# Optimization experiments

Measured on AMD Instinct MI355X. Metric: run time of the kernel, lower is better.

## Reference

```python
import jax, jax.numpy as jnp
import numpy as np

EPS = 1e-5
HEADS = 4
DIMK = 16
DIMU = 4
R = 23


def _bn_eval(x, g, b):
    # BatchNorm2d in eval mode with running_mean=0, running_var=1
    return x * (g / np.sqrt(1.0 + EPS))[None, :, None, None] + b[None, :, None, None]


def _conv1x1(x, w):
    # w: (O, C) from a Conv2d(C, O, 1) weight
    return jnp.einsum('bchw,oc->bohw', x, w)


def _lambda_layer(x, wq, wk, wv, qg, qb, vg, vb, pw, pb):
    B, C, H, W = x.shape
    n = H * W
    V = wv.shape[0] // DIMU  # dim_out // heads
    q = _bn_eval(_conv1x1(x, wq), qg, qb).reshape(B, HEADS, DIMK, n)
    k = jax.nn.softmax(_conv1x1(x, wk).reshape(B, DIMU, DIMK, n), axis=-1)
    v = _bn_eval(_conv1x1(x, wv), vg, vb).reshape(B, DIMU, V, n)
    # content lambda: (B, k, v)
    lam_c = jnp.einsum('bukn,buvn->bkv', k, v)
    y_c = jnp.einsum('bhkn,bkv->bhvn', q, lam_c)
    # position lambdas: Conv3d(u, k, (1, R, R)) == 2D conv over (H, W) with v folded into batch
    v5 = v.reshape(B, DIMU, V, H, W).transpose(0, 2, 1, 3, 4).reshape(B * V, DIMU, H, W)
    p = R // 2
    lp = jax.lax.conv_general_dilated(v5, pw, (1, 1), [(p, p), (p, p)],
                                      dimension_numbers=('NCHW', 'OIHW', 'NCHW'))
    lp = lp + pb[None, :, None, None]
    lam_p = lp.reshape(B, V, DIMK, H, W).transpose(0, 2, 1, 3, 4).reshape(B, DIMK, V, n)
    y_p = jnp.einsum('bhkn,bkvn->bhvn', q, lam_p)
    return (y_c + y_p).reshape(B, HEADS * V, H, W)


def _group_norm(x, g, b, groups=8):
    B, C, H, W = x.shape
    xr = x.reshape(B, groups, C // groups, H, W)
    m = xr.mean(axis=(2, 3, 4), keepdims=True)
    var = xr.var(axis=(2, 3, 4), keepdims=True)
    xn = ((xr - m) / jnp.sqrt(var + EPS)).reshape(B, C, H, W)
    return xn * g[None, :, None, None] + b[None, :, None, None]


def setup_inputs() -> dict:
    key = jax.random.key(0)
    B, C, H, W = 4, 64, 192, 192
    V = C // HEADS
    d = {'x': jax.random.normal(jax.random.fold_in(key, 0), (B, C, H, W), jnp.float32)}
    i = 1
    for l in (1, 2, 3):
        for nm, shape, kind in [
            ('wq', (HEADS * DIMK, C), 'w'), ('wk', (DIMU * DIMK, C), 'w'), ('wv', (DIMU * V, C), 'w'),
            ('qg', (HEADS * DIMK,), 'ones'), ('qb', (HEADS * DIMK,), 'zeros'),
            ('vg', (DIMU * V,), 'ones'), ('vb', (DIMU * V,), 'zeros'),
            ('pw', (DIMK, DIMU, R, R), 'w'), ('pb', (DIMK,), 'zeros')]:
            if kind == 'w':
                d['l%d_%s' % (l, nm)] = jax.random.normal(jax.random.fold_in(key, i), shape, jnp.float32) * 0.05
            elif kind == 'ones':
                d['l%d_%s' % (l, nm)] = jnp.ones(shape, jnp.float32)
            else:
                d['l%d_%s' % (l, nm)] = jnp.zeros(shape, jnp.float32)
            i += 1
    d['gn1_g'] = jnp.ones((C,), jnp.float32); d['gn1_b'] = jnp.zeros((C,), jnp.float32)
    d['gn3_g'] = jnp.ones((C,), jnp.float32); d['gn3_b'] = jnp.zeros((C,), jnp.float32)
    d['cw'] = jax.random.normal(jax.random.fold_in(key, 99), (C, C), jnp.float32) * 0.01
    d['cb'] = jnp.zeros((C,), jnp.float32)
    return d


def reference(x,
              l1_wq, l1_wk, l1_wv, l1_qg, l1_qb, l1_vg, l1_vb, l1_pw, l1_pb,
              l2_wq, l2_wk, l2_wv, l2_qg, l2_qb, l2_vg, l2_vb, l2_pw, l2_pb,
              l3_wq, l3_wk, l3_wv, l3_qg, l3_qb, l3_vg, l3_vb, l3_pw, l3_pb,
              gn1_g, gn1_b, gn3_g, gn3_b, cw, cb):
    out = _lambda_layer(x, l1_wq, l1_wk, l1_wv, l1_qg, l1_qb, l1_vg, l1_vb, l1_pw, l1_pb)
    out = _group_norm(out, gn1_g, gn1_b)
    out = _lambda_layer(out, l2_wq, l2_wk, l2_wv, l2_qg, l2_qb, l2_vg, l2_vb, l2_pw, l2_pb)
    out = _group_norm(out, gn1_g, gn1_b)  # original code reuses gn1 here (gn2 unused)
    out = _lambda_layer(out, l3_wq, l3_wk, l3_wv, l3_qg, l3_qb, l3_vg, l3_vb, l3_pw, l3_pb)
    out = _group_norm(out, gn3_g, gn3_b)
    out = _conv1x1(out, cw) + cb[None, :, None, None]
    return out * 0.2 + x
```

## Files before the change

kernel.cpp:

```cpp
#include <hip/hip_runtime.h>

typedef unsigned short USH;
typedef __attribute__((ext_vector_type(8))) short bf16x8;
typedef __attribute__((ext_vector_type(4))) float f32x4;

#define MFMA16(a,b,c) __builtin_amdgcn_mfma_f32_16x16x32_bf16((a),(b),(c),0,0,0)

#define BB 4
#define HH 192
#define NN 36864
#define NTOT 147456
#define CSTR 120

__device__ __forceinline__ float bf2f(USH h) {
    union { unsigned int u; float f; } v; v.u = ((unsigned int)h) << 16; return v.f;
}
__device__ __forceinline__ USH f2bf(float f) {
    union { float f; unsigned int u; } v; v.f = f;
    unsigned int u = v.u;
    return (USH)((u + 0x7FFFu + ((u >> 16) & 1u)) >> 16);
}

struct PrepArgs {
    const float* wq[3]; const float* wk[3]; const float* wv[3];
    const float* qg[3]; const float* qb[3]; const float* vg[3]; const float* vb[3];
    const float* pw[3]; const float* cw;
};
__global__ void prep_all_k(PrepArgs pa, USH* __restrict__ apc, USH* __restrict__ apq,
                           float* __restrict__ biasq, USH* __restrict__ apf) {
    int bid = blockIdx.x, tid = threadIdx.x;
    if (bid < 552) {
        int L = bid / 184, cb = bid - L * 184;
        int t = cb * 256 + tid;
        if (t < 736 * 64) {
            const float* pw = pa.pw[L];
            USH* ap = apc + (size_t)L * 376832;
            int lane = t & 63, cg = t >> 6;
            int dy = cg % 23; int ru = cg / 23; int u = ru & 3; int r = ru >> 2;
            int kk = lane & 15, q8 = (lane >> 4) * 8;
            for (int j = 0; j < 8; ++j) {
                int k = q8 + j, dx = k - r;
                USH w = 0;
                if (dx >= 0 && dx < 23) w = f2bf(pw[((kk * 4 + u) * 23 + dy) * 23 + dx]);
                ap[t * 8 + j] = w;
            }
        }
    } else if (bid < 570) {
        int idx = bid - 552; int L = idx / 6; int qblk = idx - L * 6;
        int t = qblk * 256 + tid;
        USH* apl = apq + (size_t)L * 12288;
        float* bl = biasq + L * 192;
        if (t < 1536) {
            int lane = t & 63, chunk = t >> 6;
            int mt = chunk >> 1, kc = chunk & 1;
            int o = mt * 16 + (lane & 15);
            int c0 = kc * 32 + (lane >> 4) * 8;
            float scale; const float* wrow;
            if (o < 64)       { scale = pa.qg[L][o]       * rsqrtf(1.0f + 1e-5f); wrow = pa.wq[L] + o * 64; }
            else if (o < 128) { scale = 1.0f;                                     wrow = pa.wk[L] + (o - 64) * 64; }
            else              { scale = pa.vg[L][o - 128] * rsqrtf(1.0f + 1e-5f); wrow = pa.wv[L] + (o - 128) * 64; }
            for (int j = 0; j < 8; ++j) apl[t * 8 + j] = f2bf(wrow[c0 + j] * scale);
        }
        if (t < 192) {
            float bvv;
            if (t < 64) bvv = pa.qb[L][t]; else if (t < 128) bvv = 0.0f; else bvv = pa.vb[L][t - 128];
            bl[t] = bvv;
        }
    } else {
        int t = (bid - 570) * 256 + tid;
        if (t < 512) {
            int lane = t & 63, chunk = t >> 6;
            int mt = chunk >> 1, kc = chunk & 1;
            int o = mt * 16 + (lane & 15);
            int c0 = kc * 32 + (lane >> 4) * 8;
            for (int j = 0; j < 8; ++j) apf[t * 8 + j] = f2bf(pa.cw[o * 64 + c0 + j]);
        }
    }
}

__global__ __launch_bounds__(256) void x_qkv_k(
    const float* __restrict__ xin, const bf16x8* __restrict__ apre, const float* __restrict__ bias,
    USH* __restrict__ qT, USH* __restrict__ kbuf, USH* __restrict__ vbuf) {
    __shared__ float tf[64][65];
    const int bid = blockIdx.x; const int b = bid / 576; const int nt = bid - b * 576; const int n0 = nt * 64;
    const int tid = threadIdx.x, lane = tid & 63, wq = tid >> 6;
    const int nl = lane & 15, quad = lane >> 4;
    bf16x8 afr[24];
    #pragma unroll
    for (int i = 0; i < 24; ++i) afr[i] = apre[i * 64 + lane];
    #pragma unroll
    for (int p = 0; p < 16; ++p) {
        int idx = p * 256 + tid; int c = idx >> 6, nn = idx & 63;
        tf[nn][c] = xin[((size_t)b * 64 + c) * NN + n0 + nn];
    }
    __syncthreads();
    bf16x8 b0, b1;
    #pragma unroll
    for (int j = 0; j < 8; ++j) {
        b0[j] = (short)f2bf(tf[wq * 16 + nl][quad * 8 + j]);
        b1[j] = (short)f2bf(tf[wq * 16 + nl][32 + quad * 8 + j]);
    }
    const int n = n0 + wq * 16 + nl;
    #pragma unroll
    for (int mt = 0; mt < 12; ++mt) {
        f32x4 acc = {0.f, 0.f, 0.f, 0.f};
        acc = MFMA16(afr[mt * 2 + 0], b0, acc);
        acc = MFMA16(afr[mt * 2 + 1], b1, acc);
        int o0 = mt * 16 + quad * 4;
        float4 bs = *(const float4*)(bias + o0);
        float v0 = acc[0] + bs.x, v1 = acc[1] + bs.y, v2 = acc[2] + bs.z, v3 = acc[3] + bs.w;
        if (mt < 4) {
            ushort4 pk; pk.x = f2bf(v0); pk.y = f2bf(v1); pk.z = f2bf(v2); pk.w = f2bf(v3);
            *(ushort4*)(qT + ((size_t)b * NN + n) * 64 + o0) = pk;
        } else if (mt < 8) {
            int ko = o0 - 64;
            kbuf[((size_t)b * 64 + ko    ) * NN + n] = f2bf(v0);
            kbuf[((size_t)b * 64 + ko + 1) * NN + n] = f2bf(v1);
            kbuf[((size_t)b * 64 + ko + 2) * NN + n] = f2bf(v2);
            kbuf[((size_t)b * 64 + ko + 3) * NN + n] = f2bf(v3);
        } else {
            int u = mt - 8, vv0 = quad * 4;
            vbuf[(((size_t)b * 16 + vv0    ) * 4 + u) * NN + n] = f2bf(v0);
            vbuf[(((size_t)b * 16 + vv0 + 1) * 4 + u) * NN + n] = f2bf(v1);
            vbuf[(((size_t)b * 16 + vv0 + 2) * 4 + u) * NN + n] = f2bf(v2);
            vbuf[(((size_t)b * 16 + vv0 + 3) * 4 + u) * NN + n] = f2bf(v3);
        }
    }
}

__global__ __launch_bounds__(1024) void softmax_k(USH* __restrict__ kbuf) {
    __shared__ USH row_s[NN];
    __shared__ float red[64];
    USH* p = kbuf + (size_t)blockIdx.x * NN;
    int tid = threadIdx.x, lane = tid & 63, w = tid >> 6;
    float m = -1e30f;
    for (int i = tid * 4; i < NN; i += 4096) {
        ushort4 t4 = *(const ushort4*)(p + i);
        *(ushort4*)(row_s + i) = t4;
        m = fmaxf(m, fmaxf(fmaxf(bf2f(t4.x), bf2f(t4.y)), fmaxf(bf2f(t4.z), bf2f(t4.w))));
    }
    for (int off = 32; off; off >>= 1) m = fmaxf(m, __shfl_down(m, off));
    if (lane == 0) red[w] = m;
    __syncthreads();
    if (tid == 0) { float mm = red[0]; for (int i = 1; i < 16; ++i) mm = fmaxf(mm, red[i]); red[16] = mm; }
    __syncthreads();
    float M = red[16];
    float s = 0.f;
    for (int i = tid * 4; i < NN; i += 4096) {
        ushort4 t4 = *(const ushort4*)(row_s + i);
        s += __expf(bf2f(t4.x) - M) + __expf(bf2f(t4.y) - M)
           + __expf(bf2f(t4.z) - M) + __expf(bf2f(t4.w) - M);
    }
    for (int off = 32; off; off >>= 1) s += __shfl_down(s, off);
    if (lane == 0) red[32 + w] = s;
    __syncthreads();
    if (tid == 0) { float ss = 0.f; for (int i = 0; i < 16; ++i) ss += red[32 + i]; red[17] = 1.0f / ss; }
    __syncthreads();
    float inv = red[17];
    for (int i = tid * 4; i < NN; i += 4096) {
        ushort4 t4 = *(const ushort4*)(row_s + i);
        ushort4 o4;
        o4.x = f2bf(__expf(bf2f(t4.x) - M) * inv);
        o4.y = f2bf(__expf(bf2f(t4.y) - M) * inv);
        o4.z = f2bf(__expf(bf2f(t4.z) - M) * inv);
        o4.w = f2bf(__expf(bf2f(t4.w) - M) * inv);
        *(ushort4*)(p + i) = o4;
    }
}

__global__ __launch_bounds__(64) void lamc_stage1_k(
    const USH* __restrict__ kbuf, const USH* __restrict__ vbuf,
    float* __restrict__ part) {
    int bid = blockIdx.x;
    int cidx = bid / 16; int rem = bid - cidx * 16; int b = rem >> 2; int u = rem & 3;
    int lane = threadIdx.x; int nl = lane & 15, quad = lane >> 4;
    const USH* kp = kbuf + ((size_t)b * 64 + u * 16 + nl) * NN + cidx * 1024 + quad * 8;
    const USH* vp = vbuf + (((size_t)b * 16 + nl) * 4 + u) * NN + cidx * 1024 + quad * 8;
    f32x4 acc = {0.f, 0.f, 0.f, 0.f};
    #pragma unroll 4
    for (int s = 0; s < 32; ++s) {
        bf16x8 ka = *(const bf16x8*)(kp + s * 32);
        bf16x8 va = *(const bf16x8*)(vp + s * 32);
        acc = MFMA16(ka, va, acc);
    }
    float* pout = part + ((size_t)(cidx * 4 + b) * 4 + u) * 256;
    #pragma unroll
    for (int rg = 0; rg < 4; ++rg)
        pout[nl * 16 + quad * 4 + rg] = acc[rg];
}
__global__ void lamc_stage2_k(const float* __restrict__ part, const float* __restrict__ pb,
                              float* __restrict__ lamcf) {
    int b = blockIdx.x, tid = threadIdx.x;
    float acc = 0.f;
    for (int c = 0; c < 36; ++c)
        for (int u = 0; u < 4; ++u)
            acc += part[((size_t)(c * 4 + b) * 4 + u) * 256 + tid];
    lamcf[b * 256 + tid] = acc + pb[tid & 15];
}

__global__ __launch_bounds__(256, 3) void conv_pos_fused_k(
    const USH* __restrict__ vbuf, const bf16x8* __restrict__ apre,
    const USH* __restrict__ qT, const float* __restrict__ lamcf,
    USH* __restrict__ yb, float* __restrict__ gnp2) {
    __shared__ __align__(16) USH in_s[4 * 54 * CSTR];
    __shared__ float lc_s[16];
    __shared__ float gn_s[16], gn_q[16];
    const int xh = blockIdx.x, yt = blockIdx.y, img = blockIdx.z;
    const int b = img >> 4, vvch = img & 15;
    const int tid = threadIdx.x;
    if (tid < 16) lc_s[tid] = lamcf[b * 256 + vvch * 16 + tid];
    {
        const USH* vb = vbuf + (size_t)img * 4 * NN;
        const int y0 = yt * 32 - 11, x0 = xh * 96 - 11;
        for (int idx = tid; idx < 4 * 54 * CSTR; idx += 256) {
            int u = idx / (54 * CSTR);
            int rem = idx - u * (54 * CSTR);
            int rr = rem / CSTR;
            int cc = rem - rr * CSTR;
            int gy = y0 + rr, gx = x0 + cc;
            USH val = 0;
            if (gy >= 0 && gy < HH && gx >= 0 && gx < HH) val = vb[u * NN + gy * HH + gx];
            in_s[idx] = val;
        }
    }
    __syncthreads();

    const int lane = tid & 63, wv = tid >> 6;
    const int wy = wv >> 1, wx = wv & 1;
    const int nl = lane & 15, quad = lane >> 4;
    const USH* sbase = in_s + (wy * 16 + nl) * CSTR + wx * 48 + quad * 8;
    const int ybase = yt * 32 + wy * 16 + nl;
    float lcr0 = lc_s[quad * 4], lcr1 = lc_s[quad * 4 + 1],
          lcr2 = lc_s[quad * 4 + 2], lcr3 = lc_s[quad * 4 + 3];
    const USH* qbase = qT + ((size_t)b * NN + ybase * HH) * 64 + quad * 4;
    USH* ybbase = yb + ((size_t)b * 64 + quad * 16 + vvch) * NN + ybase * HH;
    float SG = 0.f, QG = 0.f;

#define CONV_EPILOGUE(ACC, RVAL)                                                            \
    {                                                                                       \
        _Pragma("unroll")                                                                   \
        for (int xi = 0; xi < 6; ++xi) {                                                    \
            int x = xh * 96 + wx * 48 + (RVAL) + 8 * xi;                                    \
            float l0 = ACC[xi][0] + lcr0, l1 = ACC[xi][1] + lcr1;                           \
            float l2 = ACC[xi][2] + lcr2, l3 = ACC[xi][3] + lcr3;                           \
            const USH* qp = qbase + (size_t)x * 64;                                         \
            float s0, s1, s2, s3;                                                           \
            {                                                                               \
                ushort4 q4 = *(const ushort4*)(qp);                                         \
                s0 = bf2f(q4.x) * l0 + bf2f(q4.y) * l1 + bf2f(q4.z) * l2 + bf2f(q4.w) * l3; \
            }                                                                               \
            {                                                                               \
                ushort4 q4 = *(const ushort4*)(qp + 16);                                    \
                s1 = bf2f(q4.x) * l0 + bf2f(q4.y) * l1 + bf2f(q4.z) * l2 + bf2f(q4.w) * l3; \
            }                                                                               \
            {                                                                               \
                ushort4 q4 = *(const ushort4*)(qp + 32);                                    \
                s2 = bf2f(q4.x) * l0 + bf2f(q4.y) * l1 + bf2f(q4.z) * l2 + bf2f(q4.w) * l3; \
            }                                                                               \
            {                                                                               \
                ushort4 q4 = *(const ushort4*)(qp + 48);                                    \
                s3 = bf2f(q4.x) * l0 + bf2f(q4.y) * l1 + bf2f(q4.z) * l2 + bf2f(q4.w) * l3; \
            }                                                                               \
            s0 += __shfl_xor(s0, 16); s0 += __shfl_xor(s0, 32);                             \
            s1 += __shfl_xor(s1, 16); s1 += __shfl_xor(s1, 32);                             \
            s2 += __shfl_xor(s2, 16); s2 += __shfl_xor(s2, 32);                             \
            s3 += __shfl_xor(s3, 16); s3 += __shfl_xor(s3, 32);                             \
            float sel = (quad == 0) ? s0 : (quad == 1) ? s1 : (quad == 2) ? s2 : s3;        \
            USH wo = f2bf(sel);                                                             \
            ybbase[x] = wo;                                                                 \
            float wf = bf2f(wo);                                                            \
            SG += wf; QG += wf * wf;                                                        \
        }                                                                                   \
    }

#define CONV_PASS3(R0)                                                                      \
    {                                                                                       \
        f32x4 acc0[6] = {}; f32x4 acc1[6] = {}; f32x4 acc2[6] = {};                         \
        __builtin_amdgcn_s_setprio(1);                                                      \
        for (int u = 0; u < 4; ++u) {                                                       \
            const bf16x8* ap0 = apre + ((size_t)((R0) * 4 + u) * 23) * 64 + lane;           \
            const bf16x8* ap1 = ap0 + 4 * 23 * 64;                                          \
            const bf16x8* ap2 = ap0 + 2 * 4 * 23 * 64;                                      \
            const USH* srow = sbase + u * (54 * CSTR);                                      \
            _Pragma("unroll 2")                                                             \
            for (int dy = 0; dy < 23; ++dy) {                                               \
                bf16x8 a0 = *ap0, a1 = *ap1, a2 = *ap2;                                     \
                _Pragma("unroll")                                                           \
                for (int xi = 0; xi < 6; ++xi) {                                            \
                    bf16x8 bfr = *(const bf16x8*)(srow + 8 * xi);                           \
                    acc0[xi] = MFMA16(a0, bfr, acc0[xi]);                                   \
                    acc1[xi] = MFMA16(a1, bfr, acc1[xi]);                                   \
                    acc2[xi] = MFMA16(a2, bfr, acc2[xi]);                                   \
                }                                                                           \
                ap0 += 64; ap1 += 64; ap2 += 64; srow += CSTR;                               \
            }                                                                               \
        }                                                                                   \
        __builtin_amdgcn_s_setprio(0);                                                      \
        CONV_EPILOGUE(acc0, (R0))                                                           \
        CONV_EPILOGUE(acc1, (R0) + 1)                                                       \
        CONV_EPILOGUE(acc2, (R0) + 2)                                                       \
    }

    CONV_PASS3(0)
    CONV_PASS3(3)
    {
        f32x4 acc0[6] = {}; f32x4 acc1[6] = {};
        __builtin_amdgcn_s_setprio(1);
        for (int u = 0; u < 4; ++u) {
            const bf16x8* ap0 = apre + ((size_t)(6 * 4 + u) * 23) * 64 + lane;
            const bf16x8* ap1 = ap0 + 4 * 23 * 64;
            const USH* srow = sbase + u * (54 * CSTR);
            #pragma unroll 2
            for (int dy = 0; dy < 23; ++dy) {
                bf16x8 a0 = *ap0, a1 = *ap1;
                #pragma unroll
                for (int xi = 0; xi < 6; ++xi) {
                    bf16x8 bfr = *(const bf16x8*)(srow + 8 * xi);
                    acc0[xi] = MFMA16(a0, bfr, acc0[xi]);
                    acc1[xi] = MFMA16(a1, bfr, acc1[xi]);
                }
                ap0 += 64; ap1 += 64; srow += CSTR;
            }
        }
        __builtin_amdgcn_s_setprio(0);
        CONV_EPILOGUE(acc0, 6)
        CONV_EPILOGUE(acc1, 7)
    }
#undef CONV_PASS3
#undef CONV_EPILOGUE

    SG += __shfl_xor(SG, 1); SG += __shfl_xor(SG, 2); SG += __shfl_xor(SG, 4); SG += __shfl_xor(SG, 8);
    QG += __shfl_xor(QG, 1); QG += __shfl_xor(QG, 2); QG += __shfl_xor(QG, 4); QG += __shfl_xor(QG, 8);
    if (nl == 0) { gn_s[wv * 4 + quad] = SG; gn_q[wv * 4 + quad] = QG; }
    __syncthreads();
    if (tid < 4) {
        float s = gn_s[tid] + gn_s[4 + tid] + gn_s[8 + tid] + gn_s[12 + tid];
        float q = gn_q[tid] + gn_q[4 + tid] + gn_q[8 + tid] + gn_q[12 + tid];
        int lin = img * 12 + yt * 2 + xh;
        gnp2[lin * 8 + tid * 2]     = s;
        gnp2[lin * 8 + tid * 2 + 1] = q;
    }
}

__global__ void gn_passB_k(const float* __restrict__ gnp2, float* __restrict__ stats) {
    int t = threadIdx.x;
    if (t < 32) {
        int b = t >> 3, g = t & 7;
        int quad = g >> 1, v0 = (g & 1) * 8;
        float s = 0.f, q = 0.f;
        for (int vv = 0; vv < 8; ++vv)
            for (int tile = 0; tile < 12; ++tile) {
                const float* p = gnp2 + ((size_t)((b * 16 + v0 + vv) * 12 + tile)) * 8 + quad * 2;
                s += p[0]; q += p[1];
            }
        float mean = s / 294912.0f;
        float var = q / 294912.0f - mean * mean;
        stats[t * 2] = mean;
        stats[t * 2 + 1] = rsqrtf(fmaxf(var, 0.0f) + 1e-5f);
    }
}

__global__ __launch_bounds__(256) void gn_qkv_k(
    const USH* __restrict__ yb, const float* __restrict__ stats,
    const float* __restrict__ gg, const float* __restrict__ gb,
    const bf16x8* __restrict__ apre, const float* __restrict__ bias,
    USH* __restrict__ qT, USH* __restrict__ kbuf, USH* __restrict__ vbuf) {
    __shared__ float tf[64][65];
    __shared__ float sc[64], sb[64];
    const int bid = blockIdx.x; const int b = bid / 576; const int nt = bid - b * 576; const int n0 = nt * 64;
    const int tid = threadIdx.x, lane = tid & 63, wq = tid >> 6;
    const int nl = lane & 15, quad = lane >> 4;
    bf16x8 afr[24];
    #pragma unroll
    for (int i = 0; i < 24; ++i) afr[i] = apre[i * 64 + lane];
    if (tid < 64) {
        int g = tid >> 3;
        float mean = stats[(b * 8 + g) * 2], rstd = stats[(b * 8 + g) * 2 + 1];
        float ga = gg[tid];
        sc[tid] = rstd * ga;
        sb[tid] = gb[tid] - mean * rstd * ga;
    }
    __syncthreads();
    #pragma unroll
    for (int p = 0; p < 4; ++p) {
        int c = p * 16 + (tid >> 4), nn = (tid & 15) * 4;
        ushort4 y4 = *(const ushort4*)(yb + ((size_t)b * 64 + c) * NN + n0 + nn);
        float scc = sc[c], sbc = sb[c];
        tf[nn][c]     = bf2f(y4.x) * scc + sbc;
        tf[nn + 1][c] = bf2f(y4.y) * scc + sbc;
        tf[nn + 2][c] = bf2f(y4.z) * scc + sbc;
        tf[nn + 3][c] = bf2f(y4.w) * scc + sbc;
    }
    __syncthreads();
    bf16x8 b0, b1;
    #pragma unroll
    for (int j = 0; j < 8; ++j) {
        b0[j] = (short)f2bf(tf[wq * 16 + nl][quad * 8 + j]);
        b1[j] = (short)f2bf(tf[wq * 16 + nl][32 + quad * 8 + j]);
    }
    const int n = n0 + wq * 16 + nl;
    #pragma unroll
    for (int mt = 0; mt < 12; ++mt) {
        f32x4 acc = {0.f, 0.f, 0.f, 0.f};
        acc = MFMA16(afr[mt * 2 + 0], b0, acc);
        acc = MFMA16(afr[mt * 2 + 1], b1, acc);
        int o0 = mt * 16 + quad * 4;
        float4 bs = *(const float4*)(bias + o0);
        float v0 = acc[0] + bs.x, v1 = acc[1] + bs.y, v2 = acc[2] + bs.z, v3 = acc[3] + bs.w;
        if (mt < 4) {
            ushort4 pk; pk.x = f2bf(v0); pk.y = f2bf(v1); pk.z = f2bf(v2); pk.w = f2bf(v3);
            *(ushort4*)(qT + ((size_t)b * NN + n) * 64 + o0) = pk;
        } else if (mt < 8) {
            int ko = o0 - 64;
            kbuf[((size_t)b * 64 + ko    ) * NN + n] = f2bf(v0);
            kbuf[((size_t)b * 64 + ko + 1) * NN + n] = f2bf(v1);
            kbuf[((size_t)b * 64 + ko + 2) * NN + n] = f2bf(v2);
            kbuf[((size_t)b * 64 + ko + 3) * NN + n] = f2bf(v3);
        } else {
            int u = mt - 8, vv0 = quad * 4;
            vbuf[(((size_t)b * 16 + vv0    ) * 4 + u) * NN + n] = f2bf(v0);
            vbuf[(((size_t)b * 16 + vv0 + 1) * 4 + u) * NN + n] = f2bf(v1);
            vbuf[(((size_t)b * 16 + vv0 + 2) * 4 + u) * NN + n] = f2bf(v2);
            vbuf[(((size_t)b * 16 + vv0 + 3) * 4 + u) * NN + n] = f2bf(v3);
        }
    }
}

__global__ __launch_bounds__(256) void gn_final_k(
    const USH* __restrict__ yb, const float* __restrict__ stats,
    const float* __restrict__ gg, const float* __restrict__ gb,
    const bf16x8* __restrict__ apre, const float* __restrict__ cb,
    const float* __restrict__ xin, float* __restrict__ out) {
    __shared__ float tf[64][65];
    __shared__ float sc[64], sb[64];
    const int bid = blockIdx.x; const int b = bid / 576; const int nt = bid - b * 576; const int n0 = nt * 64;
    const int tid = threadIdx.x, lane = tid & 63, wq = tid >> 6;
    const int nl = lane & 15, quad = lane >> 4;
    bf16x8 afr[8];
    #pragma unroll
    for (int i = 0; i < 8; ++i) afr[i] = apre[i * 64 + lane];
    if (tid < 64) {
        int g = tid >> 3;
        float mean = stats[(b * 8 + g) * 2], rstd = stats[(b * 8 + g) * 2 + 1];
        float ga = gg[tid];
        sc[tid] = rstd * ga;
        sb[tid] = gb[tid] - mean * rstd * ga;
    }
    __syncthreads();
    #pragma unroll
    for (int p = 0; p < 4; ++p) {
        int c = p * 16 + (tid >> 4), nn = (tid & 15) * 4;
        ushort4 y4 = *(const ushort4*)(yb + ((size_t)b * 64 + c) * NN + n0 + nn);
        float scc = sc[c], sbc = sb[c];
        tf[nn][c]     = bf2f(y4.x) * scc + sbc;
        tf[nn + 1][c] = bf2f(y4.y) * scc + sbc;
        tf[nn + 2][c] = bf2f(y4.z) * scc + sbc;
        tf[nn + 3][c] = bf2f(y4.w) * scc + sbc;
    }
    __syncthreads();
    bf16x8 b0, b1;
    #pragma unroll
    for (int j = 0; j < 8; ++j) {
        b0[j] = (short)f2bf(tf[wq * 16 + nl][quad * 8 + j]);
        b1[j] = (short)f2bf(tf[wq * 16 + nl][32 + quad * 8 + j]);
    }
    const int n = n0 + wq * 16 + nl;
    #pragma unroll
    for (int mt = 0; mt < 4; ++mt) {
        f32x4 acc = {0.f, 0.f, 0.f, 0.f};
        acc = MFMA16(afr[mt * 2 + 0], b0, acc);
        acc = MFMA16(afr[mt * 2 + 1], b1, acc);
        int o0 = mt * 16 + quad * 4;
        float4 cb4 = *(const float4*)(cb + o0);
        float cbv[4] = { cb4.x, cb4.y, cb4.z, cb4.w };
        #pragma unroll
        for (int rg = 0; rg < 4; ++rg) {
            int o = o0 + rg;
            float xv = xin[((size_t)b * 64 + o) * NN + n];
            out[((size_t)b * 64 + o) * NN + n] = (acc[rg] + cbv[rg]) * 0.2f + xv;
        }
    }
}

extern "C" void kernel_launch(void* const* d_in, const int* in_sizes, int n_in,
                              void* d_out, int out_size, void* d_ws, size_t ws_size,
                              hipStream_t stream) {
    (void)in_sizes; (void)n_in; (void)out_size; (void)ws_size;
    const float* x = (const float*)d_in[0];
    char* ws = (char*)d_ws;

    const size_t SZP = (size_t)NTOT * 64 * 2;
    USH*   P0 = (USH*)(ws);
    USH*   P1 = (USH*)(ws + SZP);
    USH*   P2 = (USH*)(ws + 2 * SZP);
    USH*   P3 = (USH*)(ws + 3 * SZP);
    char*  tail  = ws + 4 * SZP;
    USH*   apc   = (USH*)(tail);            tail += 753664 * 3;
    USH*   apq   = (USH*)(tail);            tail += 24576 * 3;
    float* biasq = (float*)(tail);          tail += 768 * 3;
    USH*   apf   = (USH*)(tail);            tail += 8192;
    float* lcp   = (float*)(tail);          tail += 589824;
    float* lcf   = (float*)(tail);          tail += 4096;
    float* gnp2  = (float*)(tail);          tail += 24576;
    float* gns   = (float*)(tail);

    PrepArgs pa;
    for (int L = 0; L < 3; ++L) {
        int base = 1 + L * 9;
        pa.wq[L] = (const float*)d_in[base + 0];
        pa.wk[L] = (const float*)d_in[base + 1];
        pa.wv[L] = (const float*)d_in[base + 2];
        pa.qg[L] = (const float*)d_in[base + 3];
        pa.qb[L] = (const float*)d_in[base + 4];
        pa.vg[L] = (const float*)d_in[base + 5];
        pa.vb[L] = (const float*)d_in[base + 6];
        pa.pw[L] = (const float*)d_in[base + 7];
    }
    pa.cw = (const float*)d_in[32];

    prep_all_k<<<572, 256, 0, stream>>>(pa, apc, apq, biasq, apf);

    x_qkv_k<<<2304, 256, 0, stream>>>(x, (const bf16x8*)apq, biasq, P1, P2, P3);

    for (int L = 0; L < 3; ++L) {
        const float* pb = (const float*)d_in[1 + L * 9 + 8];
        USH* kv = (L == 1) ? P0 : P2;

        softmax_k<<<256, 1024, 0, stream>>>(kv);
        lamc_stage1_k<<<576, 64, 0, stream>>>(kv, P3, lcp);
        lamc_stage2_k<<<4, 256, 0, stream>>>(lcp, pb, lcf);
        dim3 cg(2, 6, 64);
        conv_pos_fused_k<<<cg, 256, 0, stream>>>(P3, (const bf16x8*)apc + (size_t)L * 47104,
                                                 P1, lcf, kv, gnp2);
        gn_passB_k<<<1, 256, 0, stream>>>(gnp2, gns);
        if (L < 2) {
            const float* gg = (const float*)d_in[28];
            const float* gb = (const float*)d_in[29];
            USH* knext = (L == 0) ? P0 : P2;
            gn_qkv_k<<<2304, 256, 0, stream>>>(kv, gns, gg, gb,
                                               (const bf16x8*)apq + (size_t)(L + 1) * 1536,
                                               biasq + (L + 1) * 192, P1, knext, P3);
        } else {
            const float* gg = (const float*)d_in[30];
            const float* gb = (const float*)d_in[31];
            gn_final_k<<<2304, 256, 0, stream>>>(kv, gns, gg, gb, (const bf16x8*)apf,
                                                 (const float*)d_in[33], x, (float*)d_out);
        }
    }
}
```

Before: 1.007 ms.

## Fuse softmax normalization into lambda-content MFMA and vectorize conv halo loads

The softmax kernel now only computes per-row max and reciprocal sum; the exp/normalize step is applied on the fly inside lamc_stage1, which avoids writing the normalized keys back to global memory. lamc_stage1 uses twice as many blocks with half the chunk each, and stage2 sums 72 partials. The conv halo load switches to 4-wide ushort4 loads, with the x origin and the weight pre-packing shifted by one column so the loads stay aligned. The s_setprio hints are removed. Risks: exp is now recomputed per use, and the edge check gx <= HH-4 relies on the shifted alignment to stay correct.

After: 942.1 us. 6.4% less time.

```diff
diff --git a/kernel.cpp b/kernel.cpp
--- a/kernel.cpp
+++ b/kernel.cpp
@@ -39,7 +39,7 @@
             int dy = cg % 23; int ru = cg / 23; int u = ru & 3; int r = ru >> 2;
             int kk = lane & 15, q8 = (lane >> 4) * 8;
             for (int j = 0; j < 8; ++j) {
-                int k = q8 + j, dx = k - r;
+                int k = q8 + j, dx = k - r - 1;
                 USH w = 0;
                 if (dx >= 0 && dx < 23) w = f2bf(pw[((kk * 4 + u) * 23 + dy) * 23 + dx]);
                 ap[t * 8 + j] = w;
@@ -128,10 +128,11 @@
     }
 }
 
-__global__ __launch_bounds__(1024) void softmax_k(USH* __restrict__ kbuf) {
+__global__ __launch_bounds__(1024) void softstat_k(const USH* __restrict__ kbuf,
+                                                   float* __restrict__ kstat) {
     __shared__ USH row_s[NN];
     __shared__ float red[64];
-    USH* p = kbuf + (size_t)blockIdx.x * NN;
+    const USH* p = kbuf + (size_t)blockIdx.x * NN;
     int tid = threadIdx.x, lane = tid & 63, w = tid >> 6;
     float m = -1e30f;
     for (int i = tid * 4; i < NN; i += 4096) {
@@ -154,33 +155,33 @@
     for (int off = 32; off; off >>= 1) s += __shfl_down(s, off);
     if (lane == 0) red[32 + w] = s;
     __syncthreads();
-    if (tid == 0) { float ss = 0.f; for (int i = 0; i < 16; ++i) ss += red[32 + i]; red[17] = 1.0f / ss; }
-    __syncthreads();
-    float inv = red[17];
-    for (int i = tid * 4; i < NN; i += 4096) {
-        ushort4 t4 = *(const ushort4*)(row_s + i);
-        ushort4 o4;
-        o4.x = f2bf(__expf(bf2f(t4.x) - M) * inv);
-        o4.y = f2bf(__expf(bf2f(t4.y) - M) * inv);
-        o4.z = f2bf(__expf(bf2f(t4.z) - M) * inv);
-        o4.w = f2bf(__expf(bf2f(t4.w) - M) * inv);
-        *(ushort4*)(p + i) = o4;
+    if (tid == 0) {
+        float ss = 0.f;
+        for (int i = 0; i < 16; ++i) ss += red[32 + i];
+        kstat[blockIdx.x * 2]     = M;
+        kstat[blockIdx.x * 2 + 1] = 1.0f / ss;
     }
 }
 
 __global__ __launch_bounds__(64) void lamc_stage1_k(
     const USH* __restrict__ kbuf, const USH* __restrict__ vbuf,
-    float* __restrict__ part) {
+    const float* __restrict__ kstat, float* __restrict__ part) {
     int bid = blockIdx.x;
-    int cidx = bid / 16; int rem = bid - cidx * 16; int b = rem >> 2; int u = rem & 3;
+    int cidx = bid >> 4; int rem = bid & 15; int b = rem >> 2; int u = rem & 3;
     int lane = threadIdx.x; int nl = lane & 15, quad = lane >> 4;
-    const USH* kp = kbuf + ((size_t)b * 64 + u * 16 + nl) * NN + cidx * 1024 + quad * 8;
-    const USH* vp = vbuf + (((size_t)b * 16 + nl) * 4 + u) * NN + cidx * 1024 + quad * 8;
+    int krow = b * 64 + u * 16 + nl;
+    float M = kstat[krow * 2], inv = kstat[krow * 2 + 1];
+    const USH* kp = kbuf + (size_t)krow * NN + cidx * 512 + quad * 8;
+    const USH* vp = vbuf + (((size_t)b * 16 + nl) * 4 + u) * NN + cidx * 512 + quad * 8;
     f32x4 acc = {0.f, 0.f, 0.f, 0.f};
     #pragma unroll 4
-    for (int s = 0; s < 32; ++s) {
-        bf16x8 ka = *(const bf16x8*)(kp + s * 32);
+    for (int s = 0; s < 16; ++s) {
+        bf16x8 kr = *(const bf16x8*)(kp + s * 32);
         bf16x8 va = *(const bf16x8*)(vp + s * 32);
+        bf16x8 ka;
+        #pragma unroll
+        for (int j = 0; j < 8; ++j)
+            ka[j] = (short)f2bf(__expf(bf2f((USH)kr[j]) - M) * inv);
         acc = MFMA16(ka, va, acc);
     }
     float* pout = part + ((size_t)(cidx * 4 + b) * 4 + u) * 256;
@@ -192,7 +193,7 @@
                               float* __restrict__ lamcf) {
     int b = blockIdx.x, tid = threadIdx.x;
     float acc = 0.f;
-    for (int c = 0; c < 36; ++c)
+    for (int c = 0; c < 72; ++c)
         for (int u = 0; u < 4; ++u)
             acc += part[((size_t)(c * 4 + b) * 4 + u) * 256 + tid];
     lamcf[b * 256 + tid] = acc + pb[tid & 15];
@@ -211,16 +212,17 @@
     if (tid < 16) lc_s[tid] = lamcf[b * 256 + vvch * 16 + tid];
     {
         const USH* vb = vbuf + (size_t)img * 4 * NN;
-        const int y0 = yt * 32 - 11, x0 = xh * 96 - 11;
-        for (int idx = tid; idx < 4 * 54 * CSTR; idx += 256) {
-            int u = idx / (54 * CSTR);
-            int rem = idx - u * (54 * CSTR);
-            int rr = rem / CSTR;
-            int cc = rem - rr * CSTR;
+        const int y0 = yt * 32 - 11, x0 = xh * 96 - 12;
+        for (int i4 = tid; i4 < 6480; i4 += 256) {
+            int u = i4 / 1620;
+            int rem = i4 - u * 1620;
+            int rr = rem / 30;
+            int cc = (rem - rr * 30) * 4;
             int gy = y0 + rr, gx = x0 + cc;
-            USH val = 0;
-            if (gy >= 0 && gy < HH && gx >= 0 && gx < HH) val = vb[u * NN + gy * HH + gx];
-            in_s[idx] = val;
+            ushort4 val = {0, 0, 0, 0};
+            if (gy >= 0 && gy < HH && gx >= 0 && gx <= HH - 4)
+                val = *(const ushort4*)(vb + u * NN + gy * HH + gx);
+            *(ushort4*)(in_s + (u * 54 + rr) * CSTR + cc) = val;
         }
     }
     __syncthreads();
@@ -276,7 +278,6 @@
 #define CONV_PASS3(R0)                                                                      \
     {                                                                                       \
         f32x4 acc0[6] = {}; f32x4 acc1[6] = {}; f32x4 acc2[6] = {};                         \
-        __builtin_amdgcn_s_setprio(1);                                                      \
         for (int u = 0; u < 4; ++u) {                                                       \
             const bf16x8* ap0 = apre + ((size_t)((R0) * 4 + u) * 23) * 64 + lane;           \
             const bf16x8* ap1 = ap0 + 4 * 23 * 64;                                          \
@@ -295,7 +296,6 @@
                 ap0 += 64; ap1 += 64; ap2 += 64; srow += CSTR;                               \
             }                                                                               \
         }                                                                                   \
-        __builtin_amdgcn_s_setprio(0);                                                      \
         CONV_EPILOGUE(acc0, (R0))                                                           \
         CONV_EPILOGUE(acc1, (R0) + 1)                                                       \
         CONV_EPILOGUE(acc2, (R0) + 2)                                                       \
@@ -305,7 +305,6 @@
     CONV_PASS3(3)
     {
         f32x4 acc0[6] = {}; f32x4 acc1[6] = {};
-        __builtin_amdgcn_s_setprio(1);
         for (int u = 0; u < 4; ++u) {
             const bf16x8* ap0 = apre + ((size_t)(6 * 4 + u) * 23) * 64 + lane;
             const bf16x8* ap1 = ap0 + 4 * 23 * 64;
@@ -322,7 +321,6 @@
                 ap0 += 64; ap1 += 64; srow += CSTR;
             }
         }
-        __builtin_amdgcn_s_setprio(0);
         CONV_EPILOGUE(acc0, 6)
         CONV_EPILOGUE(acc1, 7)
     }
@@ -499,10 +497,11 @@
     USH*   apq   = (USH*)(tail);            tail += 24576 * 3;
     float* biasq = (float*)(tail);          tail += 768 * 3;
     USH*   apf   = (USH*)(tail);            tail += 8192;
-    float* lcp   = (float*)(tail);          tail += 589824;
+    float* lcp   = (float*)(tail);          tail += 1179648;
     float* lcf   = (float*)(tail);          tail += 4096;
     float* gnp2  = (float*)(tail);          tail += 24576;
-    float* gns   = (float*)(tail);
+    float* gns   = (float*)(tail);          tail += 256;
+    float* kst   = (float*)(tail);
 
     PrepArgs pa;
     for (int L = 0; L < 3; ++L) {
@@ -526,8 +525,8 @@
         const float* pb = (const float*)d_in[1 + L * 9 + 8];
         USH* kv = (L == 1) ? P0 : P2;
 
-        softmax_k<<<256, 1024, 0, stream>>>(kv);
-        lamc_stage1_k<<<576, 64, 0, stream>>>(kv, P3, lcp);
+        softstat_k<<<256, 1024, 0, stream>>>(kv, kst);
+        lamc_stage1_k<<<1152, 64, 0, stream>>>(kv, P3, kst, lcp);
         lamc_stage2_k<<<4, 256, 0, stream>>>(lcp, pb, lcf);
         dim3 cg(2, 6, 64);
         conv_pos_fused_k<<<cg, 256, 0, stream>>>(P3, (const bf16x8*)apc + (size_t)L * 47104,
```
